# Performance work log

Hardware: AMD Instinct MI355X
Metric: run time of the kernel (lower is better)

Reference implementation:

```python
import jax, jax.numpy as jnp
import numpy as np

N_NODES = 50000
N_EDGES = 800000
IN_DIM, HID_DIM, OUT_DIM = 128, 128, 64


def setup_inputs() -> dict:
    key = jax.random.key(0)
    ks = jax.random.split(key, 8)
    x = jax.random.normal(ks[0], (N_NODES, IN_DIM), dtype=jnp.float32)
    edge_index = jax.random.randint(ks[1], (2, N_EDGES), 0, N_NODES, dtype=jnp.int64)
    # GCNConv uses Glorot weights + zero bias; any random init is fine for a reference
    W1 = jax.random.normal(ks[2], (IN_DIM, HID_DIM), dtype=jnp.float32) / np.sqrt(IN_DIM)
    b1 = jnp.zeros((HID_DIM,), dtype=jnp.float32)
    W2 = jax.random.normal(ks[3], (HID_DIM, OUT_DIM), dtype=jnp.float32) / np.sqrt(HID_DIM)
    b2 = jnp.zeros((OUT_DIM,), dtype=jnp.float32)
    Wfc = jax.random.normal(ks[4], (OUT_DIM, 2), dtype=jnp.float32) / np.sqrt(OUT_DIM)
    bfc = jnp.zeros((2,), dtype=jnp.float32)
    return {"x": x, "edge_index": edge_index, "W1": W1, "b1": b1,
            "W2": W2, "b2": b2, "Wfc": Wfc, "bfc": bfc}


def _gcn_conv(x, src, dst, W, b, n_nodes):
    """PyG GCNConv: out = D^{-1/2} (A+I) D^{-1/2} (x W) + b."""
    xw = x @ W  # [N, F_out] transform before propagation
    ones = jnp.ones(src.shape[0], dtype=xw.dtype)
    deg = jax.ops.segment_sum(ones, dst, num_segments=n_nodes) + 1.0  # +1 for self-loop
    dinv = jax.lax.rsqrt(deg)
    norm = dinv[src] * dinv[dst]  # [E]
    msg = xw[src] * norm[:, None]  # gather + scale: [E, F_out]
    agg = jax.ops.segment_sum(msg, dst, num_segments=n_nodes)  # scatter-add
    agg = agg + xw * (dinv * dinv)[:, None]  # self-loop contribution (norm = 1/deg)
    return agg + b


def reference(x, edge_index, W1, b1, W2, b2, Wfc, bfc):
    n = x.shape[0]
    src, dst = edge_index[0], edge_index[1]
    h = jax.nn.relu(_gcn_conv(x, src, dst, W1, b1, n))
    # dropout is identity in eval mode
    h = _gcn_conv(h, src, dst, W2, b2, n)
    h = h @ Wfc + bfc
    return jax.nn.leaky_relu(h, negative_slope=0.01)
```

## Files before the change

kernel.cpp:

```cpp
#include <hip/hip_runtime.h>
#include <hip/hip_fp16.h>

#define IN_DIM 128
#define HID_DIM 128
#define OUT_DIM 64
#define BINW 128
#define BINSHIFT 7
#define MAXBIN 512
#define EBLK 256

__global__ __launch_bounds__(256) void k_bin_hist(const int* __restrict__ dst,
                                                  int* __restrict__ hist, int E, int nbin) {
    __shared__ int h[MAXBIN];
    int tid = threadIdx.x;
    for (int k = tid; k < nbin; k += 256) h[k] = 0;
    __syncthreads();
    int per = E / gridDim.x;
    int base = blockIdx.x * per;
    int end = (blockIdx.x + 1 == gridDim.x) ? E : base + per;
    for (int i = base + tid; i < end; i += 256)
        atomicAdd(&h[dst[i] >> BINSHIFT], 1);
    __syncthreads();
    for (int k = tid; k < nbin; k += 256) hist[k * EBLK + blockIdx.x] = h[k];
}

__global__ __launch_bounds__(256) void k_bin_scan(int* __restrict__ hist,
                                                  int* __restrict__ total) {
    __shared__ int part[256];
    int k = blockIdx.x;
    int t = threadIdx.x;
    int v = hist[k * EBLK + t];
    part[t] = v;
    __syncthreads();
    for (int off = 1; off < 256; off <<= 1) {
        int u = (t >= off) ? part[t - off] : 0;
        __syncthreads();
        part[t] += u;
        __syncthreads();
    }
    hist[k * EBLK + t] = part[t] - v;
    if (t == 255) total[k] = part[255];
}

__global__ __launch_bounds__(256) void k_bin_base(const int* __restrict__ total,
                                                  int* __restrict__ bin_base, int nbin) {
    __shared__ int part[256];
    int t = threadIdx.x;
    int carry = 0;
    for (int base = 0; base < nbin; base += 256) {
        int i = base + t;
        int v = (i < nbin) ? total[i] : 0;
        part[t] = v;
        __syncthreads();
        for (int off = 1; off < 256; off <<= 1) {
            int u = (t >= off) ? part[t - off] : 0;
            __syncthreads();
            part[t] += u;
            __syncthreads();
        }
        if (i < nbin) bin_base[i] = carry + part[t] - v;
        carry += part[255];
        __syncthreads();
    }
    if (t == 0) bin_base[nbin] = carry;
}

__global__ __launch_bounds__(256) void k_bin_scatter(const int* __restrict__ src,
                                                     const int* __restrict__ dst,
                                                     const int* __restrict__ hist,
                                                     const int* __restrict__ bin_base,
                                                     unsigned int* __restrict__ ebin,
                                                     int E, int nbin) {
    __shared__ int off[MAXBIN];
    int tid = threadIdx.x;
    for (int k = tid; k < nbin; k += 256)
        off[k] = bin_base[k] + hist[k * EBLK + blockIdx.x];
    __syncthreads();
    int per = E / gridDim.x;
    int base = blockIdx.x * per;
    int end = (blockIdx.x + 1 == gridDim.x) ? E : base + per;
    for (int i = base + tid; i < end; i += 256) {
        unsigned int s = (unsigned int)src[i];
        unsigned int d = (unsigned int)dst[i];
        int pos = atomicAdd(&off[d >> BINSHIFT], 1);
        ebin[pos] = s | (d << 16);
    }
}

__global__ __launch_bounds__(256) void k_bin_fill(const unsigned int* __restrict__ ebin,
                                                  const int* __restrict__ bin_base,
                                                  int* __restrict__ row_ptr,
                                                  unsigned short* __restrict__ csr_src,
                                                  float* __restrict__ dinv, int N, int nbin) {
    __shared__ int cnt[BINW];
    __shared__ int excl[BINW];
    __shared__ int start[BINW];
    int k = blockIdx.x;
    int node0 = k * BINW;
    int nn = min(BINW, N - node0);
    int t = threadIdx.x;
    if (t < BINW) cnt[t] = 0;
    __syncthreads();
    int eb = bin_base[k], ee = bin_base[k + 1];
    for (int i = eb + t; i < ee; i += 256)
        atomicAdd(&cnt[(ebin[i] >> 16) - node0], 1);
    __syncthreads();
    if (t < BINW) excl[t] = (t < nn) ? cnt[t] : 0;
    __syncthreads();
    for (int off = 1; off < BINW; off <<= 1) {
        int u = 0;
        if (t < BINW && t >= off) u = excl[t - off];
        __syncthreads();
        if (t < BINW) excl[t] += u;
        __syncthreads();
    }
    if (t < nn) {
        int deg = cnt[t];
        int e0 = eb + excl[t] - deg;
        start[t] = e0;
        row_ptr[node0 + t] = e0;
        dinv[node0 + t] = rsqrtf((float)deg + 1.0f);
        cnt[t] = 0;
    }
    if (k == nbin - 1 && t == 0) row_ptr[N] = ee;
    __syncthreads();
    for (int i = eb + t; i < ee; i += 256) {
        unsigned int e = ebin[i];
        int dl = (int)(e >> 16) - node0;
        int slot = start[dl] + atomicAdd(&cnt[dl], 1);
        csr_src[slot] = (unsigned short)(e & 0xffffu);
    }
}

__global__ __launch_bounds__(256) void k_wc(const float* __restrict__ W2,
                                            const float* __restrict__ Wfc,
                                            const float* __restrict__ b2,
                                            const float* __restrict__ bfc,
                                            float* __restrict__ Wc,
                                            float* __restrict__ bc) {
    int t = threadIdx.x;
    int k = t >> 1, j = t & 1;
    float acc = 0.f;
#pragma unroll 8
    for (int m = 0; m < OUT_DIM; ++m) acc += W2[k * OUT_DIM + m] * Wfc[m * 2 + j];
    Wc[k * 2 + j] = acc;
    if (k == 0) {
        float b = 0.f;
#pragma unroll 8
        for (int m = 0; m < OUT_DIM; ++m) b += b2[m] * Wfc[m * 2 + j];
        bc[j] = b + bfc[j];
    }
}

__global__ __launch_bounds__(256) void k_gemm1(const float* __restrict__ x,
                                               const float* __restrict__ W,
                                               const float* __restrict__ dinv,
                                               __half* __restrict__ xwh, int N) {
    __shared__ float Ws[128][128];
    int tid = threadIdx.x;
    const float4* W4 = (const float4*)W;
    float4* Ws4 = (float4*)&Ws[0][0];
#pragma unroll
    for (int i = 0; i < 16; ++i) Ws4[tid + 256 * i] = W4[tid + 256 * i];
    __syncthreads();
    int tx = tid & 15, ty = tid >> 4;
    int row0 = blockIdx.x * 128;
    int rows[8];
    const float* xr[8];
#pragma unroll
    for (int j = 0; j < 8; ++j) {
        int row = row0 + ty + 16 * j;
        rows[j] = row;
        if (row > N - 1) row = N - 1;
        xr[j] = x + (size_t)row * IN_DIM;
    }
    float4 aclo[8], achi[8];
#pragma unroll
    for (int j = 0; j < 8; ++j) {
        aclo[j] = make_float4(0.f, 0.f, 0.f, 0.f);
        achi[j] = make_float4(0.f, 0.f, 0.f, 0.f);
    }
#pragma unroll 2
    for (int k4 = 0; k4 < 32; ++k4) {
        float4 av[8];
#pragma unroll
        for (int j = 0; j < 8; ++j) av[j] = *(const float4*)(xr[j] + k4 * 4);
#pragma unroll
        for (int kk = 0; kk < 4; ++kk) {
            float4 blo = *(const float4*)&Ws[k4 * 4 + kk][4 * tx];
            float4 bhi = *(const float4*)&Ws[k4 * 4 + kk][64 + 4 * tx];
#pragma unroll
            for (int j = 0; j < 8; ++j) {
                float a = (kk == 0) ? av[j].x : (kk == 1) ? av[j].y : (kk == 2) ? av[j].z : av[j].w;
                aclo[j].x += a * blo.x; aclo[j].y += a * blo.y;
                aclo[j].z += a * blo.z; aclo[j].w += a * blo.w;
                achi[j].x += a * bhi.x; achi[j].y += a * bhi.y;
                achi[j].z += a * bhi.z; achi[j].w += a * bhi.w;
            }
        }
    }
#pragma unroll
    for (int j = 0; j < 8; ++j) {
        if (rows[j] < N) {
            float dd = dinv[rows[j]];
            union { __half2 h[2]; uint2 u; } lo, hi;
            lo.h[0] = __floats2half2_rn(aclo[j].x * dd, aclo[j].y * dd);
            lo.h[1] = __floats2half2_rn(aclo[j].z * dd, aclo[j].w * dd);
            hi.h[0] = __floats2half2_rn(achi[j].x * dd, achi[j].y * dd);
            hi.h[1] = __floats2half2_rn(achi[j].z * dd, achi[j].w * dd);
            uint2* p = (uint2*)(xwh + (size_t)rows[j] * HID_DIM);
            p[tx] = lo.u;
            p[16 + tx] = hi.u;
        }
    }
}

__global__ __launch_bounds__(256) void k_agg1z(const int* __restrict__ row_ptr,
                                               const unsigned short* __restrict__ csr_src,
                                               const float* __restrict__ dinv,
                                               const __half* __restrict__ xwh,
                                               const float* __restrict__ b1,
                                               const float* __restrict__ Wc,
                                               float* __restrict__ z, int N) {
    constexpr int F = HID_DIM;
    constexpr int L = F / 8;
    constexpr int EPW = 64 / L;
    __shared__ float Wcs[HID_DIM * 2];
    int tid = threadIdx.x;
    if (tid < 64) ((float4*)Wcs)[tid] = ((const float4*)Wc)[tid];
    __syncthreads();
    int node = (blockIdx.x * 256 + tid) >> 6;
    if (node >= N) return;
    int lane = tid & 63;
    int sub = lane / L;
    int c   = lane % L;
    int beg = row_ptr[node], end = row_ptr[node + 1];
    float dd = dinv[node];
    uint4 us = *(const uint4*)(xwh + (size_t)node * F + c * 8);
    float4 b1a = *(const float4*)(b1 + c * 8);
    float4 b1b = *(const float4*)(b1 + c * 8 + 4);
    float a0 = 0.f, a1 = 0.f, a2 = 0.f, a3 = 0.f;
    float a4 = 0.f, a5 = 0.f, a6 = 0.f, a7 = 0.f;
    int j = beg + sub;
    for (; j + EPW < end; j += 2 * EPW) {
        int s0 = csr_src[j];
        int s1 = csr_src[j + EPW];
        uint4 u0 = *(const uint4*)(xwh + (size_t)s0 * F + c * 8);
        uint4 u1 = *(const uint4*)(xwh + (size_t)s1 * F + c * 8);
        float2 v0 = __half22float2(*(__half2*)&u0.x);
        float2 v1 = __half22float2(*(__half2*)&u0.y);
        float2 v2 = __half22float2(*(__half2*)&u0.z);
        float2 v3 = __half22float2(*(__half2*)&u0.w);
        a0 += v0.x; a1 += v0.y; a2 += v1.x; a3 += v1.y;
        a4 += v2.x; a5 += v2.y; a6 += v3.x; a7 += v3.y;
        v0 = __half22float2(*(__half2*)&u1.x);
        v1 = __half22float2(*(__half2*)&u1.y);
        v2 = __half22float2(*(__half2*)&u1.z);
        v3 = __half22float2(*(__half2*)&u1.w);
        a0 += v0.x; a1 += v0.y; a2 += v1.x; a3 += v1.y;
        a4 += v2.x; a5 += v2.y; a6 += v3.x; a7 += v3.y;
    }
    if (j < end) {
        int s = csr_src[j];
        uint4 u = *(const uint4*)(xwh + (size_t)s * F + c * 8);
        float2 v0 = __half22float2(*(__half2*)&u.x);
        float2 v1 = __half22float2(*(__half2*)&u.y);
        float2 v2 = __half22float2(*(__half2*)&u.z);
        float2 v3 = __half22float2(*(__half2*)&u.w);
        a0 += v0.x; a1 += v0.y; a2 += v1.x; a3 += v1.y;
        a4 += v2.x; a5 += v2.y; a6 += v3.x; a7 += v3.y;
    }
#pragma unroll
    for (int off = L; off < 64; off <<= 1) {
        a0 += __shfl_xor(a0, off); a1 += __shfl_xor(a1, off);
        a2 += __shfl_xor(a2, off); a3 += __shfl_xor(a3, off);
        a4 += __shfl_xor(a4, off); a5 += __shfl_xor(a5, off);
        a6 += __shfl_xor(a6, off); a7 += __shfl_xor(a7, off);
    }
    float2 v0 = __half22float2(*(__half2*)&us.x);
    float2 v1 = __half22float2(*(__half2*)&us.y);
    float2 v2 = __half22float2(*(__half2*)&us.z);
    float2 v3 = __half22float2(*(__half2*)&us.w);
    float h[8];
    h[0] = fmaxf((a0 + v0.x) * dd + b1a.x, 0.f);
    h[1] = fmaxf((a1 + v0.y) * dd + b1a.y, 0.f);
    h[2] = fmaxf((a2 + v1.x) * dd + b1a.z, 0.f);
    h[3] = fmaxf((a3 + v1.y) * dd + b1a.w, 0.f);
    h[4] = fmaxf((a4 + v2.x) * dd + b1b.x, 0.f);
    h[5] = fmaxf((a5 + v2.y) * dd + b1b.y, 0.f);
    h[6] = fmaxf((a6 + v3.x) * dd + b1b.z, 0.f);
    h[7] = fmaxf((a7 + v3.y) * dd + b1b.w, 0.f);
    float o0 = 0.f, o1 = 0.f;
#pragma unroll
    for (int k = 0; k < 8; ++k) {
        o0 += h[k] * Wcs[(c * 8 + k) * 2 + 0];
        o1 += h[k] * Wcs[(c * 8 + k) * 2 + 1];
    }
#pragma unroll
    for (int off = 1; off < L; off <<= 1) {
        o0 += __shfl_xor(o0, off);
        o1 += __shfl_xor(o1, off);
    }
    if (lane == 0) {
        float2 r; r.x = o0 * dd; r.y = o1 * dd;
        *(float2*)(z + (size_t)node * 2) = r;
    }
}

__global__ __launch_bounds__(256) void k_agg2(const int* __restrict__ row_ptr,
                                              const unsigned short* __restrict__ csr_src,
                                              const float* __restrict__ dinv,
                                              const float* __restrict__ z,
                                              const float* __restrict__ bc,
                                              float* __restrict__ out, int N) {
    int tid = threadIdx.x;
    int gwave = (blockIdx.x * 256 + tid) >> 6;
    int lane = tid & 63;
    int grp = lane >> 3, li = lane & 7;
    int node = gwave * 8 + grp;
    if (node >= N) return;
    int beg = row_ptr[node], end = row_ptr[node + 1];
    float s0 = 0.f, s1 = 0.f;
    int j = beg + li;
    for (; j + 8 < end; j += 16) {
        int sa = csr_src[j];
        int sb = csr_src[j + 8];
        float2 za = *(const float2*)(z + (size_t)sa * 2);
        float2 zb = *(const float2*)(z + (size_t)sb * 2);
        s0 += za.x + zb.x; s1 += za.y + zb.y;
    }
    if (j < end) {
        int s = csr_src[j];
        float2 zv = *(const float2*)(z + (size_t)s * 2);
        s0 += zv.x; s1 += zv.y;
    }
#pragma unroll
    for (int off = 1; off < 8; off <<= 1) {
        s0 += __shfl_xor(s0, off);
        s1 += __shfl_xor(s1, off);
    }
    if (li == 0) {
        float2 zs = *(const float2*)(z + (size_t)node * 2);
        float dd = dinv[node];
        float o0 = (s0 + zs.x) * dd + bc[0];
        float o1 = (s1 + zs.y) * dd + bc[1];
        float2 r;
        r.x = o0 > 0.f ? o0 : 0.01f * o0;
        r.y = o1 > 0.f ? o1 : 0.01f * o1;
        *(float2*)(out + (size_t)node * 2) = r;
    }
}

extern "C" void kernel_launch(void* const* d_in, const int* in_sizes, int n_in,
                              void* d_out, int out_size, void* d_ws, size_t ws_size,
                              hipStream_t stream) {
    const float* x   = (const float*)d_in[0];
    const int*   ei  = (const int*)d_in[1];
    const float* W1  = (const float*)d_in[2];
    const float* b1  = (const float*)d_in[3];
    const float* W2  = (const float*)d_in[4];
    const float* b2  = (const float*)d_in[5];
    const float* Wfc = (const float*)d_in[6];
    const float* bfc = (const float*)d_in[7];

    const int N = in_sizes[0] / IN_DIM;
    const int E = in_sizes[1] / 2;
    const int* src = ei;
    const int* dst = ei + E;
    const int nbin = (N + BINW - 1) / BINW;

    char* base = (char*)d_ws;
    size_t off = 0;
    auto take = [&](size_t bytes) { size_t o = off; off = (off + bytes + 255) & ~(size_t)255; return (void*)(base + o); };
    int*    row_ptr  = (int*)take((size_t)(N + 1) * 4);
    unsigned short* csr_src = (unsigned short*)take((size_t)E * 2);
    int*    hist     = (int*)take((size_t)nbin * EBLK * 4);
    int*    total    = (int*)take((size_t)nbin * 4);
    int*    bin_base = (int*)take((size_t)(nbin + 1) * 4);
    unsigned int* ebin = (unsigned int*)take((size_t)E * 4);
    float*  dinv     = (float*)take((size_t)N * 4);
    __half* xw1h     = (__half*)take((size_t)N * HID_DIM * 2);
    float*  zbuf     = (float*)take((size_t)N * 2 * 4);
    float*  Wc       = (float*)take((size_t)HID_DIM * 2 * 4);
    float*  bc       = (float*)take(2 * 4);

    k_bin_hist<<<EBLK, 256, 0, stream>>>(dst, hist, E, nbin);
    k_bin_scan<<<nbin, 256, 0, stream>>>(hist, total);
    k_bin_base<<<1, 256, 0, stream>>>(total, bin_base, nbin);
    k_bin_scatter<<<EBLK, 256, 0, stream>>>(src, dst, hist, bin_base, ebin, E, nbin);
    k_bin_fill<<<nbin, 256, 0, stream>>>(ebin, bin_base, row_ptr, csr_src, dinv, N, nbin);

    k_wc<<<1, 256, 0, stream>>>(W2, Wfc, b2, bfc, Wc, bc);

    const int nTile = (N + 127) / 128;

    k_gemm1<<<nTile, 256, 0, stream>>>(x, W1, dinv, xw1h, N);
    k_agg1z<<<(N + 3) / 4, 256, 0, stream>>>(row_ptr, csr_src, dinv, xw1h, b1, Wc, zbuf, N);
    const int nAgg2 = ((N + 7) / 8 * 64 + 255) / 256;
    k_agg2<<<nAgg2, 256, 0, stream>>>(row_ptr, csr_src, dinv, zbuf, bc, (float*)d_out, N);
}
```

Baseline: 178.9 us.

## Replace multi-pass CSR build with fixed-capacity per-bin buckets and overflow list

Swaps the histogram, two-level scan, scatter and fill pipeline (five kernels plus a separate Wc kernel) for one scatter kernel and one fill kernel. Each 128-node bin gets a fixed-capacity slot range claimed with global atomics, and a global overflow list catches anything past capacity. Row ends now come from a stored per-node degree, the Wc/bc precompute moves into the fill kernel, and gemm1 stages W in two 64-row halves to halve shared memory. Agg1 unrolls its gather loop four ways. The aim is to cut launch count and scan passes, at the cost of a sparse CSR layout, more workspace, and an overflow path that every fill block scans.

```diff
diff --git a/kernel.cpp b/kernel.cpp
--- a/kernel.cpp
+++ b/kernel.cpp
@@ -7,91 +7,59 @@
 #define BINW 128
 #define BINSHIFT 7
 #define MAXBIN 512
-#define EBLK 256
-
-__global__ __launch_bounds__(256) void k_bin_hist(const int* __restrict__ dst,
-                                                  int* __restrict__ hist, int E, int nbin) {
+#define CAP 4096
+#define CNTSTRIDE 16
+
+__global__ __launch_bounds__(256) void k_scatter(const int* __restrict__ src,
+                                                 const int* __restrict__ dst,
+                                                 int* __restrict__ bin_cnt,
+                                                 int* __restrict__ ovf_cnt,
+                                                 unsigned int* __restrict__ ovf,
+                                                 unsigned int* __restrict__ ebin,
+                                                 int E, int nbin) {
     __shared__ int h[MAXBIN];
-    int tid = threadIdx.x;
-    for (int k = tid; k < nbin; k += 256) h[k] = 0;
+    __shared__ int base_s[MAXBIN];
+    int t = threadIdx.x;
+    for (int k = t; k < nbin; k += 256) h[k] = 0;
     __syncthreads();
     int per = E / gridDim.x;
-    int base = blockIdx.x * per;
-    int end = (blockIdx.x + 1 == gridDim.x) ? E : base + per;
-    for (int i = base + tid; i < end; i += 256)
+    int ebeg = blockIdx.x * per;
+    int eend = (blockIdx.x + 1 == gridDim.x) ? E : ebeg + per;
+    for (int i = ebeg + t; i < eend; i += 256)
         atomicAdd(&h[dst[i] >> BINSHIFT], 1);
     __syncthreads();
-    for (int k = tid; k < nbin; k += 256) hist[k * EBLK + blockIdx.x] = h[k];
-}
-
-__global__ __launch_bounds__(256) void k_bin_scan(int* __restrict__ hist,
-                                                  int* __restrict__ total) {
-    __shared__ int part[256];
-    int k = blockIdx.x;
-    int t = threadIdx.x;
-    int v = hist[k * EBLK + t];
-    part[t] = v;
-    __syncthreads();
-    for (int off = 1; off < 256; off <<= 1) {
-        int u = (t >= off) ? part[t - off] : 0;
-        __syncthreads();
-        part[t] += u;
-        __syncthreads();
-    }
-    hist[k * EBLK + t] = part[t] - v;
-    if (t == 255) total[k] = part[255];
-}
-
-__global__ __launch_bounds__(256) void k_bin_base(const int* __restrict__ total,
-                                                  int* __restrict__ bin_base, int nbin) {
-    __shared__ int part[256];
-    int t = threadIdx.x;
-    int carry = 0;
-    for (int base = 0; base < nbin; base += 256) {
-        int i = base + t;
-        int v = (i < nbin) ? total[i] : 0;
-        part[t] = v;
-        __syncthreads();
-        for (int off = 1; off < 256; off <<= 1) {
-            int u = (t >= off) ? part[t - off] : 0;
-            __syncthreads();
-            part[t] += u;
-            __syncthreads();
-        }
-        if (i < nbin) bin_base[i] = carry + part[t] - v;
-        carry += part[255];
-        __syncthreads();
-    }
-    if (t == 0) bin_base[nbin] = carry;
-}
-
-__global__ __launch_bounds__(256) void k_bin_scatter(const int* __restrict__ src,
-                                                     const int* __restrict__ dst,
-                                                     const int* __restrict__ hist,
-                                                     const int* __restrict__ bin_base,
-                                                     unsigned int* __restrict__ ebin,
-                                                     int E, int nbin) {
-    __shared__ int off[MAXBIN];
-    int tid = threadIdx.x;
-    for (int k = tid; k < nbin; k += 256)
-        off[k] = bin_base[k] + hist[k * EBLK + blockIdx.x];
-    __syncthreads();
-    int per = E / gridDim.x;
-    int base = blockIdx.x * per;
-    int end = (blockIdx.x + 1 == gridDim.x) ? E : base + per;
-    for (int i = base + tid; i < end; i += 256) {
+    for (int k = t; k < nbin; k += 256) {
+        int c = h[k];
+        base_s[k] = (c > 0) ? atomicAdd(&bin_cnt[k * CNTSTRIDE], c) : 0;
+        h[k] = 0;
+    }
+    __syncthreads();
+    for (int i = ebeg + t; i < eend; i += 256) {
         unsigned int s = (unsigned int)src[i];
         unsigned int d = (unsigned int)dst[i];
-        int pos = atomicAdd(&off[d >> BINSHIFT], 1);
-        ebin[pos] = s | (d << 16);
-    }
-}
-
-__global__ __launch_bounds__(256) void k_bin_fill(const unsigned int* __restrict__ ebin,
-                                                  const int* __restrict__ bin_base,
-                                                  int* __restrict__ row_ptr,
-                                                  unsigned short* __restrict__ csr_src,
-                                                  float* __restrict__ dinv, int N, int nbin) {
+        int b = (int)(d >> BINSHIFT);
+        int pos = base_s[b] + atomicAdd(&h[b], 1);
+        unsigned int packed = s | (d << 16);
+        if (pos < CAP) ebin[(size_t)b * CAP + pos] = packed;
+        else ovf[atomicAdd(ovf_cnt, 1)] = packed;
+    }
+}
+
+__global__ __launch_bounds__(256) void k_fill(const unsigned int* __restrict__ ebin,
+                                              const int* __restrict__ bin_cnt,
+                                              const int* __restrict__ ovf_cnt,
+                                              const unsigned int* __restrict__ ovf,
+                                              int* __restrict__ row_ptr,
+                                              unsigned short* __restrict__ degu,
+                                              unsigned short* __restrict__ csr_src,
+                                              float* __restrict__ dinv,
+                                              const float* __restrict__ W2,
+                                              const float* __restrict__ Wfc,
+                                              const float* __restrict__ b2,
+                                              const float* __restrict__ bfc,
+                                              float* __restrict__ Wc,
+                                              float* __restrict__ bc,
+                                              int N, int nbin) {
     __shared__ int cnt[BINW];
     __shared__ int excl[BINW];
     __shared__ int start[BINW];
@@ -101,9 +69,16 @@
     int t = threadIdx.x;
     if (t < BINW) cnt[t] = 0;
     __syncthreads();
-    int eb = bin_base[k], ee = bin_base[k + 1];
-    for (int i = eb + t; i < ee; i += 256)
-        atomicAdd(&cnt[(ebin[i] >> 16) - node0], 1);
+    int cnt_k = min(bin_cnt[k * CNTSTRIDE], CAP);
+    const unsigned int* seg = ebin + (size_t)k * CAP;
+    for (int i = t; i < cnt_k; i += 256)
+        atomicAdd(&cnt[(seg[i] >> 16) & (BINW - 1)], 1);
+    int novf = *ovf_cnt;
+    for (int i = t; i < novf; i += 256) {
+        unsigned int e = ovf[i];
+        if ((int)(e >> (16 + BINSHIFT)) == k)
+            atomicAdd(&cnt[(e >> 16) & (BINW - 1)], 1);
+    }
     __syncthreads();
     if (t < BINW) excl[t] = (t < nn) ? cnt[t] : 0;
     __syncthreads();
@@ -116,39 +91,40 @@
     }
     if (t < nn) {
         int deg = cnt[t];
-        int e0 = eb + excl[t] - deg;
+        int e0 = k * CAP + excl[t] - deg;
         start[t] = e0;
         row_ptr[node0 + t] = e0;
+        degu[node0 + t] = (unsigned short)deg;
         dinv[node0 + t] = rsqrtf((float)deg + 1.0f);
         cnt[t] = 0;
     }
-    if (k == nbin - 1 && t == 0) row_ptr[N] = ee;
-    __syncthreads();
-    for (int i = eb + t; i < ee; i += 256) {
-        unsigned int e = ebin[i];
-        int dl = (int)(e >> 16) - node0;
+    __syncthreads();
+    for (int i = t; i < cnt_k; i += 256) {
+        unsigned int e = seg[i];
+        int dl = (e >> 16) & (BINW - 1);
         int slot = start[dl] + atomicAdd(&cnt[dl], 1);
         csr_src[slot] = (unsigned short)(e & 0xffffu);
     }
-}
-
-__global__ __launch_bounds__(256) void k_wc(const float* __restrict__ W2,
-                                            const float* __restrict__ Wfc,
-                                            const float* __restrict__ b2,
-                                            const float* __restrict__ bfc,
-                                            float* __restrict__ Wc,
-                                            float* __restrict__ bc) {
-    int t = threadIdx.x;
-    int k = t >> 1, j = t & 1;
-    float acc = 0.f;
+    for (int i = t; i < novf; i += 256) {
+        unsigned int e = ovf[i];
+        if ((int)(e >> (16 + BINSHIFT)) == k) {
+            int dl = (e >> 16) & (BINW - 1);
+            int slot = start[dl] + atomicAdd(&cnt[dl], 1);
+            csr_src[slot] = (unsigned short)(e & 0xffffu);
+        }
+    }
+    if (k == 0) {
+        int kk = t >> 1, j = t & 1;
+        float acc = 0.f;
 #pragma unroll 8
-    for (int m = 0; m < OUT_DIM; ++m) acc += W2[k * OUT_DIM + m] * Wfc[m * 2 + j];
-    Wc[k * 2 + j] = acc;
-    if (k == 0) {
-        float b = 0.f;
+        for (int m = 0; m < OUT_DIM; ++m) acc += W2[kk * OUT_DIM + m] * Wfc[m * 2 + j];
+        Wc[kk * 2 + j] = acc;
+        if (kk == 0) {
+            float b = 0.f;
 #pragma unroll 8
-        for (int m = 0; m < OUT_DIM; ++m) b += b2[m] * Wfc[m * 2 + j];
-        bc[j] = b + bfc[j];
+            for (int m = 0; m < OUT_DIM; ++m) b += b2[m] * Wfc[m * 2 + j];
+            bc[j] = b + bfc[j];
+        }
     }
 }
 
@@ -156,13 +132,9 @@
                                                const float* __restrict__ W,
                                                const float* __restrict__ dinv,
                                                __half* __restrict__ xwh, int N) {
-    __shared__ float Ws[128][128];
+    __shared__ float Ws[64][128];
     int tid = threadIdx.x;
-    const float4* W4 = (const float4*)W;
     float4* Ws4 = (float4*)&Ws[0][0];
-#pragma unroll
-    for (int i = 0; i < 16; ++i) Ws4[tid + 256 * i] = W4[tid + 256 * i];
-    __syncthreads();
     int tx = tid & 15, ty = tid >> 4;
     int row0 = blockIdx.x * 128;
     int rows[8];
@@ -180,24 +152,32 @@
         aclo[j] = make_float4(0.f, 0.f, 0.f, 0.f);
         achi[j] = make_float4(0.f, 0.f, 0.f, 0.f);
     }
+#pragma unroll
+    for (int ph = 0; ph < 2; ++ph) {
+        const float4* W4 = (const float4*)(W + (size_t)ph * 64 * HID_DIM);
+#pragma unroll
+        for (int i = 0; i < 8; ++i) Ws4[tid + 256 * i] = W4[tid + 256 * i];
+        __syncthreads();
 #pragma unroll 2
-    for (int k4 = 0; k4 < 32; ++k4) {
-        float4 av[8];
-#pragma unroll
-        for (int j = 0; j < 8; ++j) av[j] = *(const float4*)(xr[j] + k4 * 4);
-#pragma unroll
-        for (int kk = 0; kk < 4; ++kk) {
-            float4 blo = *(const float4*)&Ws[k4 * 4 + kk][4 * tx];
-            float4 bhi = *(const float4*)&Ws[k4 * 4 + kk][64 + 4 * tx];
-#pragma unroll
-            for (int j = 0; j < 8; ++j) {
-                float a = (kk == 0) ? av[j].x : (kk == 1) ? av[j].y : (kk == 2) ? av[j].z : av[j].w;
-                aclo[j].x += a * blo.x; aclo[j].y += a * blo.y;
-                aclo[j].z += a * blo.z; aclo[j].w += a * blo.w;
-                achi[j].x += a * bhi.x; achi[j].y += a * bhi.y;
-                achi[j].z += a * bhi.z; achi[j].w += a * bhi.w;
+        for (int k4 = 0; k4 < 16; ++k4) {
+            float4 av[8];
+#pragma unroll
+            for (int j = 0; j < 8; ++j) av[j] = *(const float4*)(xr[j] + ph * 64 + k4 * 4);
+#pragma unroll
+            for (int kk = 0; kk < 4; ++kk) {
+                float4 blo = *(const float4*)&Ws[k4 * 4 + kk][4 * tx];
+                float4 bhi = *(const float4*)&Ws[k4 * 4 + kk][64 + 4 * tx];
+#pragma unroll
+                for (int j = 0; j < 8; ++j) {
+                    float a = (kk == 0) ? av[j].x : (kk == 1) ? av[j].y : (kk == 2) ? av[j].z : av[j].w;
+                    aclo[j].x += a * blo.x; aclo[j].y += a * blo.y;
+                    aclo[j].z += a * blo.z; aclo[j].w += a * blo.w;
+                    achi[j].x += a * bhi.x; achi[j].y += a * bhi.y;
+                    achi[j].z += a * bhi.z; achi[j].w += a * bhi.w;
+                }
             }
         }
+        __syncthreads();
     }
 #pragma unroll
     for (int j = 0; j < 8; ++j) {
@@ -216,6 +196,7 @@
 }
 
 __global__ __launch_bounds__(256) void k_agg1z(const int* __restrict__ row_ptr,
+                                               const unsigned short* __restrict__ degu,
                                                const unsigned short* __restrict__ csr_src,
                                                const float* __restrict__ dinv,
                                                const __half* __restrict__ xwh,
@@ -234,41 +215,37 @@
     int lane = tid & 63;
     int sub = lane / L;
     int c   = lane % L;
-    int beg = row_ptr[node], end = row_ptr[node + 1];
+    int beg = row_ptr[node];
+    int end = beg + degu[node];
     float dd = dinv[node];
     uint4 us = *(const uint4*)(xwh + (size_t)node * F + c * 8);
     float4 b1a = *(const float4*)(b1 + c * 8);
     float4 b1b = *(const float4*)(b1 + c * 8 + 4);
     float a0 = 0.f, a1 = 0.f, a2 = 0.f, a3 = 0.f;
     float a4 = 0.f, a5 = 0.f, a6 = 0.f, a7 = 0.f;
-    int j = beg + sub;
-    for (; j + EPW < end; j += 2 * EPW) {
-        int s0 = csr_src[j];
-        int s1 = csr_src[j + EPW];
-        uint4 u0 = *(const uint4*)(xwh + (size_t)s0 * F + c * 8);
-        uint4 u1 = *(const uint4*)(xwh + (size_t)s1 * F + c * 8);
-        float2 v0 = __half22float2(*(__half2*)&u0.x);
-        float2 v1 = __half22float2(*(__half2*)&u0.y);
-        float2 v2 = __half22float2(*(__half2*)&u0.z);
-        float2 v3 = __half22float2(*(__half2*)&u0.w);
-        a0 += v0.x; a1 += v0.y; a2 += v1.x; a3 += v1.y;
-        a4 += v2.x; a5 += v2.y; a6 += v3.x; a7 += v3.y;
-        v0 = __half22float2(*(__half2*)&u1.x);
-        v1 = __half22float2(*(__half2*)&u1.y);
-        v2 = __half22float2(*(__half2*)&u1.z);
-        v3 = __half22float2(*(__half2*)&u1.w);
-        a0 += v0.x; a1 += v0.y; a2 += v1.x; a3 += v1.y;
-        a4 += v2.x; a5 += v2.y; a6 += v3.x; a7 += v3.y;
-    }
-    if (j < end) {
-        int s = csr_src[j];
-        uint4 u = *(const uint4*)(xwh + (size_t)s * F + c * 8);
+    auto acc = [&](uint4 u) {
         float2 v0 = __half22float2(*(__half2*)&u.x);
         float2 v1 = __half22float2(*(__half2*)&u.y);
         float2 v2 = __half22float2(*(__half2*)&u.z);
         float2 v3 = __half22float2(*(__half2*)&u.w);
         a0 += v0.x; a1 += v0.y; a2 += v1.x; a3 += v1.y;
         a4 += v2.x; a5 += v2.y; a6 += v3.x; a7 += v3.y;
+    };
+    int j = beg + sub;
+    for (; j + 3 * EPW < end; j += 4 * EPW) {
+        int s0 = csr_src[j];
+        int s1 = csr_src[j + EPW];
+        int s2 = csr_src[j + 2 * EPW];
+        int s3 = csr_src[j + 3 * EPW];
+        uint4 u0 = *(const uint4*)(xwh + (size_t)s0 * F + c * 8);
+        uint4 u1 = *(const uint4*)(xwh + (size_t)s1 * F + c * 8);
+        uint4 u2 = *(const uint4*)(xwh + (size_t)s2 * F + c * 8);
+        uint4 u3 = *(const uint4*)(xwh + (size_t)s3 * F + c * 8);
+        acc(u0); acc(u1); acc(u2); acc(u3);
+    }
+    for (; j < end; j += EPW) {
+        int s = csr_src[j];
+        acc(*(const uint4*)(xwh + (size_t)s * F + c * 8));
     }
 #pragma unroll
     for (int off = L; off < 64; off <<= 1) {
@@ -308,6 +285,7 @@
 }
 
 __global__ __launch_bounds__(256) void k_agg2(const int* __restrict__ row_ptr,
+                                              const unsigned short* __restrict__ degu,
                                               const unsigned short* __restrict__ csr_src,
                                               const float* __restrict__ dinv,
                                               const float* __restrict__ z,
@@ -319,7 +297,8 @@
     int grp = lane >> 3, li = lane & 7;
     int node = gwave * 8 + grp;
     if (node >= N) return;
-    int beg = row_ptr[node], end = row_ptr[node + 1];
+    int beg = row_ptr[node];
+    int end = beg + degu[node];
     float s0 = 0.f, s1 = 0.f;
     int j = beg + li;
     for (; j + 8 < end; j += 16) {
@@ -372,30 +351,29 @@
     char* base = (char*)d_ws;
     size_t off = 0;
     auto take = [&](size_t bytes) { size_t o = off; off = (off + bytes + 255) & ~(size_t)255; return (void*)(base + o); };
-    int*    row_ptr  = (int*)take((size_t)(N + 1) * 4);
-    unsigned short* csr_src = (unsigned short*)take((size_t)E * 2);
-    int*    hist     = (int*)take((size_t)nbin * EBLK * 4);
-    int*    total    = (int*)take((size_t)nbin * 4);
-    int*    bin_base = (int*)take((size_t)(nbin + 1) * 4);
-    unsigned int* ebin = (unsigned int*)take((size_t)E * 4);
+    int*    row_ptr  = (int*)take((size_t)N * 4);
+    unsigned short* degu = (unsigned short*)take((size_t)N * 2);
+    unsigned short* csr_src = (unsigned short*)take((size_t)nbin * CAP * 2);
+    int*    bin_cnt  = (int*)take((size_t)(nbin * CNTSTRIDE + CNTSTRIDE) * 4);
+    int*    ovf_cnt  = bin_cnt + nbin * CNTSTRIDE;
+    unsigned int* ovf = (unsigned int*)take((size_t)E * 4);
+    unsigned int* ebin = (unsigned int*)take((size_t)nbin * CAP * 4);
     float*  dinv     = (float*)take((size_t)N * 4);
     __half* xw1h     = (__half*)take((size_t)N * HID_DIM * 2);
     float*  zbuf     = (float*)take((size_t)N * 2 * 4);
     float*  Wc       = (float*)take((size_t)HID_DIM * 2 * 4);
     float*  bc       = (float*)take(2 * 4);
 
-    k_bin_hist<<<EBLK, 256, 0, stream>>>(dst, hist, E, nbin);
-    k_bin_scan<<<nbin, 256, 0, stream>>>(hist, total);
-    k_bin_base<<<1, 256, 0, stream>>>(total, bin_base, nbin);
-    k_bin_scatter<<<EBLK, 256, 0, stream>>>(src, dst, hist, bin_base, ebin, E, nbin);
-    k_bin_fill<<<nbin, 256, 0, stream>>>(ebin, bin_base, row_ptr, csr_src, dinv, N, nbin);
-
-    k_wc<<<1, 256, 0, stream>>>(W2, Wfc, b2, bfc, Wc, bc);
+    hipMemsetAsync(bin_cnt, 0, (size_t)(nbin * CNTSTRIDE + CNTSTRIDE) * 4, stream);
+
+    k_scatter<<<256, 256, 0, stream>>>(src, dst, bin_cnt, ovf_cnt, ovf, ebin, E, nbin);
+    k_fill<<<nbin, 256, 0, stream>>>(ebin, bin_cnt, ovf_cnt, ovf, row_ptr, degu,
+                                     csr_src, dinv, W2, Wfc, b2, bfc, Wc, bc, N, nbin);
 
     const int nTile = (N + 127) / 128;
 
     k_gemm1<<<nTile, 256, 0, stream>>>(x, W1, dinv, xw1h, N);
-    k_agg1z<<<(N + 3) / 4, 256, 0, stream>>>(row_ptr, csr_src, dinv, xw1h, b1, Wc, zbuf, N);
+    k_agg1z<<<(N + 3) / 4, 256, 0, stream>>>(row_ptr, degu, csr_src, dinv, xw1h, b1, Wc, zbuf, N);
     const int nAgg2 = ((N + 7) / 8 * 64 + 255) / 256;
-    k_agg2<<<nAgg2, 256, 0, stream>>>(row_ptr, csr_src, dinv, zbuf, bc, (float*)d_out, N);
-}
+    k_agg2<<<nAgg2, 256, 0, stream>>>(row_ptr, degu, csr_src, dinv, zbuf, bc, (float*)d_out, N);
+}
```

Result: no change. 178.1 us (median of 2 runs) (-0.5%).
